# Performance work log

Measured on AMD Instinct MI355X. Metric: run time of the kernel, lower is better.

## Reference

```python
import jax, jax.numpy as jnp
import numpy as np

SEQ, SUB, B, V = 32, 16, 512, 258
U = SEQ // SUB
Z, CH, CO, DH = 512, 1024, 512, 1024


def _lstm_cell(x, h, c, Wi, Wh, bi, bh):
    # torch gate order: input, forget, cell, output
    g = x @ Wi + h @ Wh + bi + bh  # [B, 4H]
    i, f, gg, o = jnp.split(g, 4, axis=-1)
    c = jax.nn.sigmoid(f) * c + jax.nn.sigmoid(i) * jnp.tanh(gg)
    h = jax.nn.sigmoid(o) * jnp.tanh(c)
    return h, c


def _lstm2(xs, h1_0, p1, p2):
    # xs: [T,B,in]; h1_0: [B,H] layer-1 initial hidden.
    # Layer-2 hidden and both cell states start at zero (initialize_state in torch code).
    z0 = jnp.zeros_like(h1_0)
    def step(carry, x):
        h1, c1, h2, c2 = carry
        h1, c1 = _lstm_cell(x, h1, c1, *p1)
        h2, c2 = _lstm_cell(h1, h2, c2, *p2)
        return (h1, c1, h2, c2), h2
    _, hs = jax.lax.scan(step, (h1_0, z0, z0, z0), xs)
    return hs  # [T,B,H] top-layer hidden states


def setup_inputs() -> dict:
    key = jax.random.key(0)
    ks = iter(jax.random.split(key, 40))
    def w(shape, s=0.05):
        return jax.random.normal(next(ks), shape, dtype=jnp.float32) * s
    return {
        "z": jax.random.normal(next(ks), (B, Z), dtype=jnp.float32),
        "x": jax.random.uniform(next(ks), (SEQ, B, V), dtype=jnp.float32),
        "conductor_input": w((1, B, V)),
        "ci_W": w((Z, CH)), "ci_b": w((CH,)),
        "cW1i": w((V, 4 * CH)), "cW1h": w((CH, 4 * CH)), "cb1i": w((4 * CH,)), "cb1h": w((4 * CH,)),
        "cW2i": w((CH, 4 * CH)), "cW2h": w((CH, 4 * CH)), "cb2i": w((4 * CH,)), "cb2h": w((4 * CH,)),
        "co_W": w((CH, CO)), "co_b": w((CO,)),
        "di_W": w((CO, DH)), "di_b": w((DH,)),
        "dW1i": w((CO + V, 4 * DH)), "dW1h": w((DH, 4 * DH)), "db1i": w((4 * DH,)), "db1h": w((4 * DH,)),
        "dW2i": w((DH, 4 * DH)), "dW2h": w((DH, 4 * DH)), "db2i": w((4 * DH,)), "db2h": w((4 * DH,)),
        "fc_W": w((DH, V)), "fc_b": w((V,)),
    }


def reference(z, x, conductor_input, ci_W, ci_b, cW1i, cW1h, cb1i, cb1h, cW2i, cW2h, cb2i, cb2h, co_W, co_b, di_W, di_b, dW1i, dW1h, db1i, db1h, dW2i, dW2h, db2i, db2h, fc_W, fc_b):
    # --- conductor: 2-layer LSTM over U steps of a learned constant input ---
    h1 = jnp.tanh(z @ ci_W + ci_b)  # [B,CH] layer-1 init hidden
    cin = jnp.broadcast_to(conductor_input, (U, B, V))
    ch = _lstm2(cin, h1, (cW1i, cW1h, cb1i, cb1h), (cW2i, cW2h, cb2i, cb2h))  # [U,B,CH]
    c = ch @ co_W + co_b  # [U,B,CO]
    # --- decoder (teacher forcing): state resets each sub-sequence, so the U
    # segments of length SUB are independent given c -> vmap over segments ---
    sos = jnp.zeros((1, B, V), jnp.float32).at[:, :, 0].set(1.0)
    prev = jnp.concatenate([sos, x[:-1]], axis=0).reshape(U, SUB, B, V)
    cb = jnp.broadcast_to(c[:, None], (U, SUB, B, CO))
    dec_in = jnp.concatenate([cb, prev], axis=-1)  # [U,SUB,B,CO+V]
    def run_seg(xs, cj):
        h1_0 = jnp.tanh(cj @ di_W + di_b)  # [B,DH]
        return _lstm2(xs, h1_0, (dW1i, dW1h, db1i, db1h), (dW2i, dW2h, db2i, db2h))
    hs = jax.vmap(run_seg)(dec_in, c)  # [U,SUB,B,DH]
    logp = jax.nn.log_softmax(hs @ fc_W + fc_b, axis=-1)  # log(softmax(.)) fused
    return logp.reshape(SEQ, B, V).transpose(1, 0, 2)  # [B,SEQ,V]
```

## Files before the change

kernel.cpp:

```cpp
#include <hip/hip_runtime.h>
#include <cstddef>
#include <cstdint>


namespace {

typedef short s8v __attribute__((ext_vector_type(8)));
typedef float f4v __attribute__((ext_vector_type(4)));
typedef unsigned short ushort_t;

__device__ inline unsigned short f2bf(float f) {
    union { float f; unsigned u; } v; v.f = f;
    unsigned r = v.u + 0x7fff + ((v.u >> 16) & 1);
    return (unsigned short)(r >> 16);
}
__device__ inline float bf2f(ushort_t u) {
    union { unsigned u; float f; } v; v.u = ((unsigned)u) << 16; return v.f;
}
__device__ inline float sigm_f(float x) { return 1.f / (1.f + __expf(-x)); }
__device__ inline float tanh_f(float x) {
    const float e = __expf(2.f * fabsf(x));
    return copysignf(1.f - 2.f / (e + 1.f), x);
}

#define GLOAD_LDS(gp, lp)                                              \
    __builtin_amdgcn_global_load_lds(                                  \
        (const __attribute__((address_space(1))) void*)(gp),           \
        (__attribute__((address_space(3))) void*)(lp), 16, 0, 0)

__device__ __forceinline__ void gemm_core(
    const ushort_t* __restrict__ A1a, const ushort_t* __restrict__ A1b,
    int lda1, int K1, const ushort_t* __restrict__ B1t,
    const ushort_t* __restrict__ A2, int lda2, int K2,
    const ushort_t* __restrict__ B2t,
    int bm, int bn, ushort_t* lds, f4v acc[4][4])
{
    const int tid = threadIdx.x;
    const int wid = tid >> 6;
    const int lane = tid & 63;

    const int sr0 = wid * 16 + (lane >> 2);
    const int sr1 = sr0 + 64;
    const int rl0 = sr0 ^ ((sr0 >> 2) & 1);
    const int rl1 = sr1 ^ ((sr1 >> 2) & 1);
    const int c0 = (((lane & 3) ^ (rl0 & 3)) << 3);
    const int c1 = (((lane & 3) ^ (rl1 & 3)) << 3);
    const int ldst = wid * 512;

    auto arow = [&](const ushort_t* Aa, const ushort_t* Ab, int lda,
                    int r) -> const ushort_t* {
        return (Ab != nullptr && r >= 512) ? Ab + (size_t)(r - 512) * lda
                                           : Aa + (size_t)r * lda;
    };
    const ushort_t* a1r0 = arow(A1a, A1b, lda1, bm + rl0) + c0;
    const ushort_t* a1r1 = arow(A1a, A1b, lda1, bm + rl1) + c1;
    const ushort_t* b1r0 = B1t + (size_t)(bn + rl0) * K1 + c0;
    const ushort_t* b1r1 = B1t + (size_t)(bn + rl1) * K1 + c1;
    const int n1 = K1 >> 5, n2 = (B2t != nullptr) ? (K2 >> 5) : 0;
    const int nt = n1 + n2;
    const ushort_t* a2r0 = nullptr; const ushort_t* a2r1 = nullptr;
    const ushort_t* b2r0 = nullptr; const ushort_t* b2r1 = nullptr;
    if (n2 > 0) {
        a2r0 = A2 + (size_t)(bm + rl0) * lda2 + c0;
        a2r1 = A2 + (size_t)(bm + rl1) * lda2 + c1;
        b2r0 = B2t + (size_t)(bn + rl0) * K2 + c0;
        b2r1 = B2t + (size_t)(bn + rl1) * K2 + c1;
    }

    auto stage = [&](int idx, int buf) {
        ushort_t* Lb = lds + buf * 8192;
        const ushort_t *pa0, *pa1, *pb0, *pb1;
        if (idx < n1) {
            const int k0 = idx << 5;
            pa0 = a1r0 + k0; pa1 = a1r1 + k0; pb0 = b1r0 + k0; pb1 = b1r1 + k0;
        } else {
            const int k0 = (idx - n1) << 5;
            pa0 = a2r0 + k0; pa1 = a2r1 + k0; pb0 = b2r0 + k0; pb1 = b2r1 + k0;
        }
        GLOAD_LDS(pa0, Lb + ldst);
        GLOAD_LDS(pa1, Lb + 2048 + ldst);
        GLOAD_LDS(pb0, Lb + 4096 + ldst);
        GLOAD_LDS(pb1, Lb + 6144 + ldst);
    };

    const int wr = wid >> 1, wc = wid & 1;
    const int lrow = lane & 15, lkg = lane >> 4;
    int aoff[4], boff[4];
#pragma unroll
    for (int m = 0; m < 4; ++m) {
        const int r = wr * 64 + m * 16 + lrow;
        aoff[m] = (r ^ ((r >> 2) & 1)) * 32 + ((lkg ^ (r & 3)) << 3);
    }
#pragma unroll
    for (int n = 0; n < 4; ++n) {
        const int r = wc * 64 + n * 16 + lrow;
        boff[n] = 4096 + (r ^ ((r >> 2) & 1)) * 32 + ((lkg ^ (r & 3)) << 3);
    }

    stage(0, 0);
    stage(1, 1);
    int sbuf = 2, cbuf = 0;
    for (int t = 0; t < nt; ++t) {
        if (t == nt - 1) {
            asm volatile("s_waitcnt vmcnt(0)" ::: "memory");
        } else {
            asm volatile("s_waitcnt vmcnt(4)" ::: "memory");
        }
        __builtin_amdgcn_s_barrier();
        __builtin_amdgcn_sched_barrier(0);
        if (t + 2 < nt) {
            stage(t + 2, sbuf);
            sbuf = (sbuf == 2) ? 0 : sbuf + 1;
        }
        const ushort_t* L = lds + cbuf * 8192;
        s8v af[4], bv[4];
#pragma unroll
        for (int m = 0; m < 4; ++m) af[m] = *(const s8v*)(L + aoff[m]);
#pragma unroll
        for (int n = 0; n < 4; ++n) bv[n] = *(const s8v*)(L + boff[n]);
        __builtin_amdgcn_s_setprio(1);
#pragma unroll
        for (int m = 0; m < 4; ++m)
#pragma unroll
            for (int n = 0; n < 4; ++n)
                acc[m][n] = __builtin_amdgcn_mfma_f32_16x16x32_bf16(
                    af[m], bv[n], acc[m][n], 0, 0, 0);
        __builtin_amdgcn_s_setprio(0);
        cbuf = (cbuf == 2) ? 0 : cbuf + 1;
    }
}

template <int ACT>
__global__ __launch_bounds__(256) void plain_gemm(
    const ushort_t* __restrict__ A, int lda, int K,
    const ushort_t* __restrict__ Bt,
    const float* __restrict__ bias, int bias_n,
    float* __restrict__ C, ushort_t* __restrict__ Cbf, int N)
{
    __shared__ __align__(16) ushort_t lds[3 * 8192];
    const int bm = blockIdx.x * 128, bn = blockIdx.y * 128;
    f4v acc[4][4] = {};
    gemm_core(A, nullptr, lda, K, Bt, nullptr, 0, 0, nullptr, bm, bn, lds, acc);

    const int tid = threadIdx.x, wid = tid >> 6, lane = tid & 63;
    const int wr = wid >> 1, wc = wid & 1, lrow = lane & 15, lkg = lane >> 4;
#pragma unroll
    for (int m = 0; m < 4; ++m) {
        const int row0 = bm + wr * 64 + m * 16 + lkg * 4;
#pragma unroll
        for (int n = 0; n < 4; ++n) {
            const int col = bn + wc * 64 + n * 16 + lrow;
            const float bv = (bias != nullptr && col < bias_n) ? bias[col] : 0.f;
#pragma unroll
            for (int r = 0; r < 4; ++r) {
                float v = acc[m][n][r] + bv;
                if (ACT == 1) v = tanh_f(v);
                const size_t o = (size_t)(row0 + r) * N + col;
                if (C != nullptr) C[o] = v;
                if (Cbf != nullptr) Cbf[o] = f2bf(v);
            }
        }
    }
}

struct Prob {
    const ushort_t* A1a; const ushort_t* A1b; int lda1; int K1;
    const ushort_t* B1t;
    const ushort_t* A2; int lda2; int K2; const ushort_t* B2t;
    const ushort_t* Dbf;
    const float* bias;
    float* cst;
    ushort_t* hout;
    ushort_t* hs;
    int step_s;
};

__global__ __launch_bounds__(256) void lstm_step(Prob PA, int nxa, Prob PB,
                                                 int mshift)
{
    __shared__ __align__(16) ushort_t lds[3 * 8192];
    const int nblk = gridDim.x;
    const int wg = blockIdx.x;
    const int swz = (wg & 7) * (nblk >> 3) + (wg >> 3);
    const int nmb = 1 << mshift;
    const int nb = swz >> mshift;
    const int mb = swz & (nmb - 1);

    const bool isA = mb < nxa;
    const Prob& P = isA ? PA : PB;
    const int bm = (isA ? mb : mb - nxa) * 128;
    const int bn = nb * 128;

    f4v acc[4][4] = {};
    gemm_core(P.A1a, P.A1b, P.lda1, P.K1, P.B1t,
              P.A2, P.lda2, P.K2, P.B2t, bm, bn, lds, acc);

    const int tid = threadIdx.x, wid = tid >> 6, lane = tid & 63;
    const int wr = wid >> 1, wc = wid & 1, lrow = lane & 15, lkg = lane >> 4;
    const int colbase = bn + wc * 64;
    const int jb = (colbase >> 6) * 16 + lrow;

#pragma unroll
    for (int m = 0; m < 4; ++m) {
        const int row0 = bm + wr * 64 + m * 16 + lkg * 4;
#pragma unroll
        for (int r = 0; r < 4; ++r) {
            const int row = row0 + r;
            float g0 = acc[m][0][r], g1 = acc[m][1][r];
            float g2 = acc[m][2][r], g3 = acc[m][3][r];
            if (P.Dbf != nullptr) {
                const ushort_t* d = P.Dbf + (size_t)row * 4096 + colbase + lrow;
                g0 += bf2f(d[0]); g1 += bf2f(d[16]);
                g2 += bf2f(d[32]); g3 += bf2f(d[48]);
            }
            if (P.bias != nullptr) {
                const float* b = P.bias + colbase + lrow;
                g0 += b[0]; g1 += b[16]; g2 += b[32]; g3 += b[48];
            }
            const size_t ci = (size_t)row * 1024 + jb;
            const float cn = fmaf(sigm_f(g1), P.cst[ci], sigm_f(g0) * tanh_f(g2));
            const float hn = sigm_f(g3) * tanh_f(cn);
            P.cst[ci] = cn;
            const ushort_t hb = f2bf(hn);
            P.hout[ci] = hb;
            if (P.hs != nullptr) {
                size_t d;
                if (P.step_s >= 0) {
                    const int u = row >> 9, b = row & 511;
                    d = ((size_t)((u * 16 + P.step_s) * 512 + b) << 10) + jb;
                } else {
                    d = ci;
                }
                P.hs[d] = hb;
            }
        }
    }
}

template <int PERM>
__global__ __launch_bounds__(256) void transpose_to_bf16(
    const float* __restrict__ in, ushort_t* __restrict__ out,
    int K, int N, int Kp, int Np)
{
    __shared__ float tile[32][33];
    const int k0 = blockIdx.x * 32, n0 = blockIdx.y * 32;
    const int tx = threadIdx.x, ty = threadIdx.y;
#pragma unroll
    for (int q = 0; q < 4; ++q) {
        const int k = k0 + ty + 8 * q, n = n0 + tx;
        tile[ty + 8 * q][tx] = (k < K && n < N) ? in[(size_t)k * N + n] : 0.f;
    }
    __syncthreads();
#pragma unroll
    for (int q = 0; q < 4; ++q) {
        const int n = n0 + ty + 8 * q, k = k0 + tx;
        int np = n;
        if (PERM) np = ((n & 1023) >> 4) * 64 + (n >> 10) * 16 + (n & 15);
        out[(size_t)np * Kp + k] = f2bf(tile[tx][ty + 8 * q]);
    }
}

__global__ void convert_pad_bf16(const float* __restrict__ in,
                                 ushort_t* __restrict__ out,
                                 int K, int Kp, int total)
{
    const int idx = blockIdx.x * 256 + threadIdx.x;
    if (idx >= total) return;
    const int r = idx / Kp, k = idx - r * Kp;
    out[idx] = (k < K) ? f2bf(in[(size_t)r * K + k]) : (ushort_t)0;
}

__global__ void sos_init_bf16(ushort_t* __restrict__ sos)
{
    const int i = blockIdx.x * 256 + threadIdx.x;
    if (i < 512 * 288) sos[i] = ((i % 288) == 0) ? (ushort_t)0x3F80 : (ushort_t)0;
}

__global__ void permute_bias(const float* __restrict__ b1,
                             const float* __restrict__ b2,
                             float* __restrict__ out)
{
    const int c = blockIdx.x * 256 + threadIdx.x;
    if (c >= 4096) return;
    const int g = (c >> 4) & 3;
    const int j = (c >> 6) * 16 + (c & 15);
    out[c] = b1[g * 1024 + j] + b2[g * 1024 + j];
}

__global__ __launch_bounds__(256) void logsoftmax_kernel(
    const float* __restrict__ logits, float* __restrict__ out)
{
    const int row = blockIdx.x;
    const int tid = threadIdx.x;
    const float* L = logits + (size_t)row * 384;
    const int t = row >> 9;
    const int b = row & 511;
    float* O = out + ((size_t)b * 32 + t) * 258;

    const float x0 = L[tid];
    const float x1 = (tid < 2) ? L[256 + tid] : -1e30f;

    __shared__ float sm[4];
    float m = fmaxf(x0, x1);
#pragma unroll
    for (int off = 32; off > 0; off >>= 1) m = fmaxf(m, __shfl_down(m, off));
    if ((tid & 63) == 0) sm[tid >> 6] = m;
    __syncthreads();
    m = fmaxf(fmaxf(sm[0], sm[1]), fmaxf(sm[2], sm[3]));
    __syncthreads();

    float s = expf(x0 - m) + ((tid < 2) ? expf(x1 - m) : 0.f);
#pragma unroll
    for (int off = 32; off > 0; off >>= 1) s += __shfl_down(s, off);
    if ((tid & 63) == 0) sm[tid >> 6] = s;
    __syncthreads();
    s = sm[0] + sm[1] + sm[2] + sm[3];

    const float lse = m + logf(s);
    O[tid] = x0 - lse;
    if (tid < 2) O[256 + tid] = x1 - lse;
}

}

extern "C" void kernel_launch(void* const* d_in, const int* in_sizes, int n_in,
                              void* d_out, int out_size, void* d_ws, size_t ws_size,
                              hipStream_t stream)
{
    (void)in_sizes; (void)n_in; (void)out_size; (void)ws_size;

    const float* z    = (const float*)d_in[0];
    const float* x    = (const float*)d_in[1];
    const float* cin  = (const float*)d_in[2];
    const float* ciW  = (const float*)d_in[3];
    const float* cib  = (const float*)d_in[4];
    const float* cW1i = (const float*)d_in[5];
    const float* cW1h = (const float*)d_in[6];
    const float* cb1i = (const float*)d_in[7];
    const float* cb1h = (const float*)d_in[8];
    const float* cW2i = (const float*)d_in[9];
    const float* cW2h = (const float*)d_in[10];
    const float* cb2i = (const float*)d_in[11];
    const float* cb2h = (const float*)d_in[12];
    const float* coW  = (const float*)d_in[13];
    const float* cob  = (const float*)d_in[14];
    const float* diW  = (const float*)d_in[15];
    const float* dib  = (const float*)d_in[16];
    const float* dW1i = (const float*)d_in[17];
    const float* dW1h = (const float*)d_in[18];
    const float* db1i = (const float*)d_in[19];
    const float* db1h = (const float*)d_in[20];
    const float* dW2i = (const float*)d_in[21];
    const float* dW2h = (const float*)d_in[22];
    const float* db2i = (const float*)d_in[23];
    const float* db2h = (const float*)d_in[24];
    const float* fcW  = (const float*)d_in[25];
    const float* fcb  = (const float*)d_in[26];
    float* out = (float*)d_out;

    char* wsp = (char*)d_ws;
    size_t off = 0;
    auto allocf = [&](size_t n) { float* p = (float*)(wsp + off); off += n * 4; return p; };
    auto allocb = [&](size_t n) { ushort_t* p = (ushort_t*)(wsp + off); off += n * 2; return p; };

    float* cst = allocf((size_t)3 * 1024 * 1024 + 64);
    float* c1c = cst;
    float* c2c = cst + (size_t)512 * 1024;
    float* c1d = cst + (size_t)1024 * 1024;
    float* c2d = cst + (size_t)2 * 1024 * 1024;
    float* pb1c = allocf(4096);
    float* pb2c = allocf(4096);
    float* pb1d = allocf(4096);
    float* pb2d = allocf(4096);
    float* logits = allocf((size_t)16384 * 384);

    ushort_t* h2z  = allocb((size_t)2 * (512 + 1024) * 1024);
    ushort_t* hc2A = h2z;
    ushort_t* hc2B = h2z + (size_t)512 * 1024;
    ushort_t* h2dA = h2z + (size_t)2 * 512 * 1024;
    ushort_t* h2dB = h2z + (size_t)(2 * 512 + 1024) * 1024;

    ushort_t* hc1A = allocb((size_t)512 * 1024);
    ushort_t* hc1B = allocb((size_t)512 * 1024);
    ushort_t* h1dA = allocb((size_t)1024 * 1024);
    ushort_t* h1dB = allocb((size_t)1024 * 1024);

    ushort_t* zbf    = allocb((size_t)512 * 512);
    ushort_t* cinbf  = allocb((size_t)512 * 288);
    ushort_t* sosbf  = allocb((size_t)512 * 288);
    ushort_t* xbf    = allocb((size_t)16384 * 288);
    ushort_t* chbf   = allocb((size_t)1024 * 1024);
    ushort_t* ccode  = allocb((size_t)1024 * 512);
    ushort_t* cpre   = allocb((size_t)1024 * 4096);
    ushort_t* xW1c   = allocb((size_t)512 * 4096);
    ushort_t* hsbf   = allocb((size_t)16384 * 1024);

    ushort_t* ciWt  = allocb((size_t)1024 * 512);
    ushort_t* cW1it = allocb((size_t)4096 * 288);
    ushort_t* cW1ht = allocb((size_t)4096 * 1024);
    ushort_t* cW2it = allocb((size_t)4096 * 1024);
    ushort_t* cW2ht = allocb((size_t)4096 * 1024);
    ushort_t* coWt  = allocb((size_t)512 * 1024);
    ushort_t* dtopt = allocb((size_t)4096 * 512);
    ushort_t* dbott = allocb((size_t)4096 * 288);
    ushort_t* diWt  = allocb((size_t)1024 * 512);
    ushort_t* dW1ht = allocb((size_t)4096 * 1024);
    ushort_t* dW2it = allocb((size_t)4096 * 1024);
    ushort_t* dW2ht = allocb((size_t)4096 * 1024);
    ushort_t* fcWt  = allocb((size_t)384 * 1024);

    hipMemsetAsync(cst, 0, (size_t)3 * 1024 * 1024 * 4, stream);
    hipMemsetAsync(h2z, 0, (size_t)2 * (512 + 1024) * 1024 * 2, stream);

    auto transp = [&](const float* in, ushort_t* o, int K, int N, int Kp, int Np, int perm) {
        dim3 g(Kp / 32, Np / 32), b(32, 8);
        if (perm) transpose_to_bf16<1><<<g, b, 0, stream>>>(in, o, K, N, Kp, Np);
        else      transpose_to_bf16<0><<<g, b, 0, stream>>>(in, o, K, N, Kp, Np);
    };
    transp(ciW, ciWt, 512, 1024, 512, 1024, 0);
    transp(cW1i, cW1it, 258, 4096, 288, 4096, 1);
    transp(cW1h, cW1ht, 1024, 4096, 1024, 4096, 1);
    transp(cW2i, cW2it, 1024, 4096, 1024, 4096, 1);
    transp(cW2h, cW2ht, 1024, 4096, 1024, 4096, 1);
    transp(coW, coWt, 1024, 512, 1024, 512, 0);
    transp(dW1i, dtopt, 512, 4096, 512, 4096, 1);
    transp(dW1i + (size_t)512 * 4096, dbott, 258, 4096, 288, 4096, 1);
    transp(diW, diWt, 512, 1024, 512, 1024, 0);
    transp(dW1h, dW1ht, 1024, 4096, 1024, 4096, 1);
    transp(dW2i, dW2it, 1024, 4096, 1024, 4096, 1);
    transp(dW2h, dW2ht, 1024, 4096, 1024, 4096, 1);
    transp(fcW, fcWt, 1024, 258, 1024, 384, 0);

    auto convert = [&](const float* in, ushort_t* o, int K, int Kp, int R) {
        const int total = R * Kp;
        convert_pad_bf16<<<dim3((total + 255) / 256), 256, 0, stream>>>(in, o, K, Kp, total);
    };
    convert(z, zbf, 512, 512, 512);
    convert(cin, cinbf, 258, 288, 512);
    convert(x, xbf, 258, 288, 16384);
    sos_init_bf16<<<dim3((512 * 288 + 255) / 256), 256, 0, stream>>>(sosbf);
    permute_bias<<<16, 256, 0, stream>>>(cb1i, cb1h, pb1c);
    permute_bias<<<16, 256, 0, stream>>>(cb2i, cb2h, pb2c);
    permute_bias<<<16, 256, 0, stream>>>(db1i, db1h, pb1d);
    permute_bias<<<16, 256, 0, stream>>>(db2i, db2h, pb2d);

    auto gemm = [&](int act, const ushort_t* A, int lda, int K, const ushort_t* Bt,
                    const float* bias, int bias_n,
                    float* C, ushort_t* Cbf, int M, int N) {
        dim3 g(M / 128, N / 128);
        if (act) plain_gemm<1><<<g, 256, 0, stream>>>(A, lda, K, Bt, bias, bias_n, C, Cbf, N);
        else     plain_gemm<0><<<g, 256, 0, stream>>>(A, lda, K, Bt, bias, bias_n, C, Cbf, N);
    };

    gemm(1, zbf, 512, 512, ciWt, cib, 1024, nullptr, hc1A, 512, 1024);
    gemm(0, cinbf, 288, 288, cW1it, pb1c, 4096, nullptr, xW1c, 512, 4096);

    ushort_t* HC1[2] = {hc1A, hc1B};
    ushort_t* HC2[2] = {hc2A, hc2B};
    for (int k = 0; k <= 2; ++k) {
        Prob pa{}, pb{};
        int nxa = 0, nxb = 0;
        if (k < 2) {
            pa = {HC1[k & 1], nullptr, 1024, 1024, cW1ht,
                  nullptr, 0, 0, nullptr,
                  xW1c, nullptr, c1c, HC1[(k + 1) & 1], nullptr, -1};
            nxa = 4;
        }
        if (k >= 1) {
            pb = {HC1[k & 1], nullptr, 1024, 1024, cW2it,
                  HC2[k & 1], 1024, 1024, cW2ht,
                  nullptr, pb2c, c2c, HC2[(k + 1) & 1],
                  chbf + (size_t)(k - 1) * 512 * 1024, -1};
            nxb = 4;
        }
        const int nmb = nxa + nxb;
        const int mshift = (nmb == 4) ? 2 : 3;
        lstm_step<<<dim3(nmb * 32), 256, 0, stream>>>(pa, nxa, pb, mshift);
    }

    gemm(0, chbf, 1024, 1024, coWt, cob, 512, nullptr, ccode, 1024, 512);
    gemm(0, ccode, 512, 512, dtopt, pb1d, 4096, nullptr, cpre, 1024, 4096);
    gemm(1, ccode, 512, 512, diWt, dib, 1024, nullptr, h1dA, 1024, 1024);

    ushort_t* H1[2] = {h1dA, h1dB};
    ushort_t* H2[2] = {h2dA, h2dB};
    for (int k = 0; k <= 16; ++k) {
        Prob pa{}, pb{};
        int nxa = 0, nxb = 0;
        if (k < 16) {
            const ushort_t* plo = (k == 0) ? sosbf : (xbf + (size_t)(k - 1) * 512 * 288);
            const ushort_t* phi = xbf + (size_t)(15 + k) * 512 * 288;
            pa = {plo, phi, 288, 288, dbott,
                  H1[k & 1], 1024, 1024, dW1ht,
                  cpre, nullptr, c1d, H1[(k + 1) & 1], nullptr, -1};
            nxa = 8;
        }
        if (k >= 1) {
            pb = {H1[k & 1], nullptr, 1024, 1024, dW2it,
                  H2[k & 1], 1024, 1024, dW2ht,
                  nullptr, pb2d, c2d, H2[(k + 1) & 1], hsbf, k - 1};
            nxb = 8;
        }
        const int nmb = nxa + nxb;
        const int mshift = (nmb == 8) ? 3 : 4;
        lstm_step<<<dim3(nmb * 32), 256, 0, stream>>>(pa, nxa, pb, mshift);
    }

    gemm(0, hsbf, 1024, 1024, fcWt, fcb, 258, logits, nullptr, 16384, 384);
    logsoftmax_kernel<<<dim3(16384), 256, 0, stream>>>(logits, out);
}
```

Baseline: 1.108 ms.

## Enlarge GEMM tiles to 128x256 with K=64 stages and XOR-swizzled LDS

Changes the shared GEMM core from 128x128 tiles with a K step of 32 to 128x256 tiles with a K step of 64. Staging uses row-wise global-to-LDS loads and an 8-chunk XOR swizzle, and the LSTM and plain GEMM launches halve their column-block count. The padded K of the 258-wide inputs grows from 288 to 320, and the logits width from 384 to 512, so dimensions stay multiples of the new tile sizes. This aims to raise MFMA work per LDS load and cut redundant A-tile fetches. In exchange, LDS use and register pressure rise (launch bounds of one block), grids shrink so fewer CUs are busy on the small recurrent steps, and the padding adds wasted work.

```diff
diff --git a/kernel.cpp b/kernel.cpp
--- a/kernel.cpp
+++ b/kernel.cpp
@@ -27,119 +27,114 @@
     __builtin_amdgcn_global_load_lds(                                  \
         (const __attribute__((address_space(1))) void*)(gp),           \
         (__attribute__((address_space(3))) void*)(lp), 16, 0, 0)
+
+constexpr int kBufElems = 24576;
 
 __device__ __forceinline__ void gemm_core(
     const ushort_t* __restrict__ A1a, const ushort_t* __restrict__ A1b,
     int lda1, int K1, const ushort_t* __restrict__ B1t,
     const ushort_t* __restrict__ A2, int lda2, int K2,
     const ushort_t* __restrict__ B2t,
-    int bm, int bn, ushort_t* lds, f4v acc[4][4])
+    int bm, int bn, ushort_t* lds, f4v acc[4][8])
 {
     const int tid = threadIdx.x;
     const int wid = tid >> 6;
     const int lane = tid & 63;
 
-    const int sr0 = wid * 16 + (lane >> 2);
-    const int sr1 = sr0 + 64;
-    const int rl0 = sr0 ^ ((sr0 >> 2) & 1);
-    const int rl1 = sr1 ^ ((sr1 >> 2) & 1);
-    const int c0 = (((lane & 3) ^ (rl0 & 3)) << 3);
-    const int c1 = (((lane & 3) ^ (rl1 & 3)) << 3);
-    const int ldst = wid * 512;
-
-    auto arow = [&](const ushort_t* Aa, const ushort_t* Ab, int lda,
-                    int r) -> const ushort_t* {
-        return (Ab != nullptr && r >= 512) ? Ab + (size_t)(r - 512) * lda
-                                           : Aa + (size_t)r * lda;
-    };
-    const ushort_t* a1r0 = arow(A1a, A1b, lda1, bm + rl0) + c0;
-    const ushort_t* a1r1 = arow(A1a, A1b, lda1, bm + rl1) + c1;
-    const ushort_t* b1r0 = B1t + (size_t)(bn + rl0) * K1 + c0;
-    const ushort_t* b1r1 = B1t + (size_t)(bn + rl1) * K1 + c1;
-    const int n1 = K1 >> 5, n2 = (B2t != nullptr) ? (K2 >> 5) : 0;
+    const int srow8 = lane >> 3;
+    const int schunk = (lane & 7) ^ srow8;
+
+    const int n1 = K1 >> 6;
+    const int n2 = (B2t != nullptr) ? (K2 >> 6) : 0;
     const int nt = n1 + n2;
-    const ushort_t* a2r0 = nullptr; const ushort_t* a2r1 = nullptr;
-    const ushort_t* b2r0 = nullptr; const ushort_t* b2r1 = nullptr;
+
+    const ushort_t* Ab1 = (A1b != nullptr && bm >= 512)
+                              ? A1b + (size_t)(bm - 512) * lda1
+                              : A1a + (size_t)bm * lda1;
+    const ushort_t* pA1 = Ab1 + (size_t)(wid * 32 + srow8) * lda1 + schunk * 8;
+    const ushort_t* pB1 = B1t + (size_t)(bn + wid * 64 + srow8) * K1 + schunk * 8;
+    const ushort_t* pA2 = nullptr;
+    const ushort_t* pB2 = nullptr;
     if (n2 > 0) {
-        a2r0 = A2 + (size_t)(bm + rl0) * lda2 + c0;
-        a2r1 = A2 + (size_t)(bm + rl1) * lda2 + c1;
-        b2r0 = B2t + (size_t)(bn + rl0) * K2 + c0;
-        b2r1 = B2t + (size_t)(bn + rl1) * K2 + c1;
+        pA2 = A2 + (size_t)(bm + wid * 32 + srow8) * lda2 + schunk * 8;
+        pB2 = B2t + (size_t)(bn + wid * 64 + srow8) * K2 + schunk * 8;
     }
 
     auto stage = [&](int idx, int buf) {
-        ushort_t* Lb = lds + buf * 8192;
-        const ushort_t *pa0, *pa1, *pb0, *pb1;
-        if (idx < n1) {
-            const int k0 = idx << 5;
-            pa0 = a1r0 + k0; pa1 = a1r1 + k0; pb0 = b1r0 + k0; pb1 = b1r1 + k0;
-        } else {
-            const int k0 = (idx - n1) << 5;
-            pa0 = a2r0 + k0; pa1 = a2r1 + k0; pb0 = b2r0 + k0; pb1 = b2r1 + k0;
-        }
-        GLOAD_LDS(pa0, Lb + ldst);
-        GLOAD_LDS(pa1, Lb + 2048 + ldst);
-        GLOAD_LDS(pb0, Lb + 4096 + ldst);
-        GLOAD_LDS(pb1, Lb + 6144 + ldst);
+        ushort_t* Lb = lds + buf * kBufElems;
+        const ushort_t *pa, *pb;
+        size_t la, lb;
+        if (idx < n1) { pa = pA1 + (idx << 6); pb = pB1 + (idx << 6); la = lda1; lb = K1; }
+        else { const int i2 = idx - n1; pa = pA2 + (i2 << 6); pb = pB2 + (i2 << 6); la = lda2; lb = K2; }
+#pragma unroll
+        for (int j = 0; j < 4; ++j)
+            GLOAD_LDS(pa + (size_t)(j * 8) * la, Lb + (wid * 32 + j * 8) * 64);
+#pragma unroll
+        for (int j = 0; j < 8; ++j)
+            GLOAD_LDS(pb + (size_t)(j * 8) * lb, Lb + 8192 + (wid * 64 + j * 8) * 64);
     };
 
     const int wr = wid >> 1, wc = wid & 1;
     const int lrow = lane & 15, lkg = lane >> 4;
-    int aoff[4], boff[4];
+    int aoff[4][2], boff[8][2];
 #pragma unroll
     for (int m = 0; m < 4; ++m) {
         const int r = wr * 64 + m * 16 + lrow;
-        aoff[m] = (r ^ ((r >> 2) & 1)) * 32 + ((lkg ^ (r & 3)) << 3);
-    }
-#pragma unroll
-    for (int n = 0; n < 4; ++n) {
-        const int r = wc * 64 + n * 16 + lrow;
-        boff[n] = 4096 + (r ^ ((r >> 2) & 1)) * 32 + ((lkg ^ (r & 3)) << 3);
+#pragma unroll
+        for (int s = 0; s < 2; ++s)
+            aoff[m][s] = r * 64 + (((s * 4 + lkg) ^ (r & 7)) << 3);
+    }
+#pragma unroll
+    for (int n = 0; n < 8; ++n) {
+        const int r = wc * 128 + n * 16 + lrow;
+#pragma unroll
+        for (int s = 0; s < 2; ++s)
+            boff[n][s] = 8192 + r * 64 + (((s * 4 + lkg) ^ (r & 7)) << 3);
     }
 
     stage(0, 0);
-    stage(1, 1);
+    if (nt > 1) stage(1, 1);
     int sbuf = 2, cbuf = 0;
     for (int t = 0; t < nt; ++t) {
-        if (t == nt - 1) {
-            asm volatile("s_waitcnt vmcnt(0)" ::: "memory");
-        } else {
-            asm volatile("s_waitcnt vmcnt(4)" ::: "memory");
-        }
+        if (t + 1 < nt) asm volatile("s_waitcnt vmcnt(12)" ::: "memory");
+        else            asm volatile("s_waitcnt vmcnt(0)" ::: "memory");
         __builtin_amdgcn_s_barrier();
         __builtin_amdgcn_sched_barrier(0);
         if (t + 2 < nt) {
             stage(t + 2, sbuf);
             sbuf = (sbuf == 2) ? 0 : sbuf + 1;
         }
-        const ushort_t* L = lds + cbuf * 8192;
-        s8v af[4], bv[4];
-#pragma unroll
-        for (int m = 0; m < 4; ++m) af[m] = *(const s8v*)(L + aoff[m]);
-#pragma unroll
-        for (int n = 0; n < 4; ++n) bv[n] = *(const s8v*)(L + boff[n]);
-        __builtin_amdgcn_s_setprio(1);
-#pragma unroll
-        for (int m = 0; m < 4; ++m)
-#pragma unroll
-            for (int n = 0; n < 4; ++n)
-                acc[m][n] = __builtin_amdgcn_mfma_f32_16x16x32_bf16(
-                    af[m], bv[n], acc[m][n], 0, 0, 0);
-        __builtin_amdgcn_s_setprio(0);
+        const ushort_t* L = lds + cbuf * kBufElems;
+#pragma unroll
+        for (int s = 0; s < 2; ++s) {
+            s8v a[4], b[8];
+#pragma unroll
+            for (int m = 0; m < 4; ++m) a[m] = *(const s8v*)(L + aoff[m][s]);
+#pragma unroll
+            for (int n = 0; n < 8; ++n) b[n] = *(const s8v*)(L + boff[n][s]);
+            __builtin_amdgcn_s_setprio(1);
+#pragma unroll
+            for (int m = 0; m < 4; ++m)
+#pragma unroll
+                for (int n = 0; n < 8; ++n)
+                    acc[m][n] = __builtin_amdgcn_mfma_f32_16x16x32_bf16(
+                        a[m], b[n], acc[m][n], 0, 0, 0);
+            __builtin_amdgcn_s_setprio(0);
+        }
         cbuf = (cbuf == 2) ? 0 : cbuf + 1;
     }
 }
 
 template <int ACT>
-__global__ __launch_bounds__(256) void plain_gemm(
+__global__ __launch_bounds__(256, 1) void plain_gemm(
     const ushort_t* __restrict__ A, int lda, int K,
     const ushort_t* __restrict__ Bt,
     const float* __restrict__ bias, int bias_n,
     float* __restrict__ C, ushort_t* __restrict__ Cbf, int N)
 {
-    __shared__ __align__(16) ushort_t lds[3 * 8192];
-    const int bm = blockIdx.x * 128, bn = blockIdx.y * 128;
-    f4v acc[4][4] = {};
+    __shared__ __align__(16) ushort_t lds[3 * kBufElems];
+    const int bm = blockIdx.x * 128, bn = blockIdx.y * 256;
+    f4v acc[4][8] = {};
     gemm_core(A, nullptr, lda, K, Bt, nullptr, 0, 0, nullptr, bm, bn, lds, acc);
 
     const int tid = threadIdx.x, wid = tid >> 6, lane = tid & 63;
@@ -148,8 +143,8 @@
     for (int m = 0; m < 4; ++m) {
         const int row0 = bm + wr * 64 + m * 16 + lkg * 4;
 #pragma unroll
-        for (int n = 0; n < 4; ++n) {
-            const int col = bn + wc * 64 + n * 16 + lrow;
+        for (int n = 0; n < 8; ++n) {
+            const int col = bn + wc * 128 + n * 16 + lrow;
             const float bv = (bias != nullptr && col < bias_n) ? bias[col] : 0.f;
 #pragma unroll
             for (int r = 0; r < 4; ++r) {
@@ -175,10 +170,10 @@
     int step_s;
 };
 
-__global__ __launch_bounds__(256) void lstm_step(Prob PA, int nxa, Prob PB,
-                                                 int mshift)
-{
-    __shared__ __align__(16) ushort_t lds[3 * 8192];
+__global__ __launch_bounds__(256, 1) void lstm_step(Prob PA, int nxa, Prob PB,
+                                                    int mshift)
+{
+    __shared__ __align__(16) ushort_t lds[3 * kBufElems];
     const int nblk = gridDim.x;
     const int wg = blockIdx.x;
     const int swz = (wg & 7) * (nblk >> 3) + (wg >> 3);
@@ -189,49 +184,52 @@
     const bool isA = mb < nxa;
     const Prob& P = isA ? PA : PB;
     const int bm = (isA ? mb : mb - nxa) * 128;
-    const int bn = nb * 128;
-
-    f4v acc[4][4] = {};
+    const int bn = nb * 256;
+
+    f4v acc[4][8] = {};
     gemm_core(P.A1a, P.A1b, P.lda1, P.K1, P.B1t,
               P.A2, P.lda2, P.K2, P.B2t, bm, bn, lds, acc);
 
     const int tid = threadIdx.x, wid = tid >> 6, lane = tid & 63;
     const int wr = wid >> 1, wc = wid & 1, lrow = lane & 15, lkg = lane >> 4;
-    const int colbase = bn + wc * 64;
-    const int jb = (colbase >> 6) * 16 + lrow;
-
-#pragma unroll
-    for (int m = 0; m < 4; ++m) {
-        const int row0 = bm + wr * 64 + m * 16 + lkg * 4;
-#pragma unroll
-        for (int r = 0; r < 4; ++r) {
-            const int row = row0 + r;
-            float g0 = acc[m][0][r], g1 = acc[m][1][r];
-            float g2 = acc[m][2][r], g3 = acc[m][3][r];
-            if (P.Dbf != nullptr) {
-                const ushort_t* d = P.Dbf + (size_t)row * 4096 + colbase + lrow;
-                g0 += bf2f(d[0]); g1 += bf2f(d[16]);
-                g2 += bf2f(d[32]); g3 += bf2f(d[48]);
-            }
-            if (P.bias != nullptr) {
-                const float* b = P.bias + colbase + lrow;
-                g0 += b[0]; g1 += b[16]; g2 += b[32]; g3 += b[48];
-            }
-            const size_t ci = (size_t)row * 1024 + jb;
-            const float cn = fmaf(sigm_f(g1), P.cst[ci], sigm_f(g0) * tanh_f(g2));
-            const float hn = sigm_f(g3) * tanh_f(cn);
-            P.cst[ci] = cn;
-            const ushort_t hb = f2bf(hn);
-            P.hout[ci] = hb;
-            if (P.hs != nullptr) {
-                size_t d;
-                if (P.step_s >= 0) {
-                    const int u = row >> 9, b = row & 511;
-                    d = ((size_t)((u * 16 + P.step_s) * 512 + b) << 10) + jb;
-                } else {
-                    d = ci;
+
+#pragma unroll
+    for (int nn = 0; nn < 2; ++nn) {
+        const int colbase = bn + wc * 128 + nn * 64;
+        const int jb = (colbase >> 6) * 16 + lrow;
+#pragma unroll
+        for (int m = 0; m < 4; ++m) {
+            const int row0 = bm + wr * 64 + m * 16 + lkg * 4;
+#pragma unroll
+            for (int r = 0; r < 4; ++r) {
+                const int row = row0 + r;
+                float g0 = acc[m][nn * 4 + 0][r], g1 = acc[m][nn * 4 + 1][r];
+                float g2 = acc[m][nn * 4 + 2][r], g3 = acc[m][nn * 4 + 3][r];
+                if (P.Dbf != nullptr) {
+                    const ushort_t* d = P.Dbf + (size_t)row * 4096 + colbase + lrow;
+                    g0 += bf2f(d[0]); g1 += bf2f(d[16]);
+                    g2 += bf2f(d[32]); g3 += bf2f(d[48]);
                 }
-                P.hs[d] = hb;
+                if (P.bias != nullptr) {
+                    const float* b = P.bias + colbase + lrow;
+                    g0 += b[0]; g1 += b[16]; g2 += b[32]; g3 += b[48];
+                }
+                const size_t ci = (size_t)row * 1024 + jb;
+                const float cn = fmaf(sigm_f(g1), P.cst[ci], sigm_f(g0) * tanh_f(g2));
+                const float hn = sigm_f(g3) * tanh_f(cn);
+                P.cst[ci] = cn;
+                const ushort_t hb = f2bf(hn);
+                P.hout[ci] = hb;
+                if (P.hs != nullptr) {
+                    size_t d;
+                    if (P.step_s >= 0) {
+                        const int u = row >> 9, b = row & 511;
+                        d = ((size_t)((u * 16 + P.step_s) * 512 + b) << 10) + jb;
+                    } else {
+                        d = ci;
+                    }
+                    P.hs[d] = hb;
+                }
             }
         }
     }
@@ -273,7 +271,7 @@
 __global__ void sos_init_bf16(ushort_t* __restrict__ sos)
 {
     const int i = blockIdx.x * 256 + threadIdx.x;
-    if (i < 512 * 288) sos[i] = ((i % 288) == 0) ? (ushort_t)0x3F80 : (ushort_t)0;
+    if (i < 512 * 320) sos[i] = ((i % 320) == 0) ? (ushort_t)0x3F80 : (ushort_t)0;
 }
 
 __global__ void permute_bias(const float* __restrict__ b1,
@@ -292,7 +290,7 @@
 {
     const int row = blockIdx.x;
     const int tid = threadIdx.x;
-    const float* L = logits + (size_t)row * 384;
+    const float* L = logits + (size_t)row * 512;
     const int t = row >> 9;
     const int b = row & 511;
     float* O = out + ((size_t)b * 32 + t) * 258;
@@ -372,7 +370,7 @@
     float* pb2c = allocf(4096);
     float* pb1d = allocf(4096);
     float* pb2d = allocf(4096);
-    float* logits = allocf((size_t)16384 * 384);
+    float* logits = allocf((size_t)16384 * 512);
 
     ushort_t* h2z  = allocb((size_t)2 * (512 + 1024) * 1024);
     ushort_t* hc2A = h2z;
@@ -386,9 +384,9 @@
     ushort_t* h1dB = allocb((size_t)1024 * 1024);
 
     ushort_t* zbf    = allocb((size_t)512 * 512);
-    ushort_t* cinbf  = allocb((size_t)512 * 288);
-    ushort_t* sosbf  = allocb((size_t)512 * 288);
-    ushort_t* xbf    = allocb((size_t)16384 * 288);
+    ushort_t* cinbf  = allocb((size_t)512 * 320);
+    ushort_t* sosbf  = allocb((size_t)512 * 320);
+    ushort_t* xbf    = allocb((size_t)16384 * 320);
     ushort_t* chbf   = allocb((size_t)1024 * 1024);
     ushort_t* ccode  = allocb((size_t)1024 * 512);
     ushort_t* cpre   = allocb((size_t)1024 * 4096);
@@ -396,18 +394,18 @@
     ushort_t* hsbf   = allocb((size_t)16384 * 1024);
 
     ushort_t* ciWt  = allocb((size_t)1024 * 512);
-    ushort_t* cW1it = allocb((size_t)4096 * 288);
+    ushort_t* cW1it = allocb((size_t)4096 * 320);
     ushort_t* cW1ht = allocb((size_t)4096 * 1024);
     ushort_t* cW2it = allocb((size_t)4096 * 1024);
     ushort_t* cW2ht = allocb((size_t)4096 * 1024);
     ushort_t* coWt  = allocb((size_t)512 * 1024);
     ushort_t* dtopt = allocb((size_t)4096 * 512);
-    ushort_t* dbott = allocb((size_t)4096 * 288);
+    ushort_t* dbott = allocb((size_t)4096 * 320);
     ushort_t* diWt  = allocb((size_t)1024 * 512);
     ushort_t* dW1ht = allocb((size_t)4096 * 1024);
     ushort_t* dW2it = allocb((size_t)4096 * 1024);
     ushort_t* dW2ht = allocb((size_t)4096 * 1024);
-    ushort_t* fcWt  = allocb((size_t)384 * 1024);
+    ushort_t* fcWt  = allocb((size_t)512 * 1024);
 
     hipMemsetAsync(cst, 0, (size_t)3 * 1024 * 1024 * 4, stream);
     hipMemsetAsync(h2z, 0, (size_t)2 * (512 + 1024) * 1024 * 2, stream);
@@ -418,27 +416,27 @@
         else      transpose_to_bf16<0><<<g, b, 0, stream>>>(in, o, K, N, Kp, Np);
     };
     transp(ciW, ciWt, 512, 1024, 512, 1024, 0);
-    transp(cW1i, cW1it, 258, 4096, 288, 4096, 1);
+    transp(cW1i, cW1it, 258, 4096, 320, 4096, 1);
     transp(cW1h, cW1ht, 1024, 4096, 1024, 4096, 1);
     transp(cW2i, cW2it, 1024, 4096, 1024, 4096, 1);
     transp(cW2h, cW2ht, 1024, 4096, 1024, 4096, 1);
     transp(coW, coWt, 1024, 512, 1024, 512, 0);
     transp(dW1i, dtopt, 512, 4096, 512, 4096, 1);
-    transp(dW1i + (size_t)512 * 4096, dbott, 258, 4096, 288, 4096, 1);
+    transp(dW1i + (size_t)512 * 4096, dbott, 258, 4096, 320, 4096, 1);
     transp(diW, diWt, 512, 1024, 512, 1024, 0);
     transp(dW1h, dW1ht, 1024, 4096, 1024, 4096, 1);
     transp(dW2i, dW2it, 1024, 4096, 1024, 4096, 1);
     transp(dW2h, dW2ht, 1024, 4096, 1024, 4096, 1);
-    transp(fcW, fcWt, 1024, 258, 1024, 384, 0);
+    transp(fcW, fcWt, 1024, 258, 1024, 512, 0);
 
     auto convert = [&](const float* in, ushort_t* o, int K, int Kp, int R) {
         const int total = R * Kp;
         convert_pad_bf16<<<dim3((total + 255) / 256), 256, 0, stream>>>(in, o, K, Kp, total);
     };
     convert(z, zbf, 512, 512, 512);
-    convert(cin, cinbf, 258, 288, 512);
-    convert(x, xbf, 258, 288, 16384);
-    sos_init_bf16<<<dim3((512 * 288 + 255) / 256), 256, 0, stream>>>(sosbf);
+    convert(cin, cinbf, 258, 320, 512);
+    convert(x, xbf, 258, 320, 16384);
+    sos_init_bf16<<<dim3((512 * 320 + 255) / 256), 256, 0, stream>>>(sosbf);
     permute_bias<<<16, 256, 0, stream>>>(cb1i, cb1h, pb1c);
     permute_bias<<<16, 256, 0, stream>>>(cb2i, cb2h, pb2c);
     permute_bias<<<16, 256, 0, stream>>>(db1i, db1h, pb1d);
@@ -447,13 +445,13 @@
     auto gemm = [&](int act, const ushort_t* A, int lda, int K, const ushort_t* Bt,
                     const float* bias, int bias_n,
                     float* C, ushort_t* Cbf, int M, int N) {
-        dim3 g(M / 128, N / 128);
+        dim3 g(M / 128, N / 256);
         if (act) plain_gemm<1><<<g, 256, 0, stream>>>(A, lda, K, Bt, bias, bias_n, C, Cbf, N);
         else     plain_gemm<0><<<g, 256, 0, stream>>>(A, lda, K, Bt, bias, bias_n, C, Cbf, N);
     };
 
     gemm(1, zbf, 512, 512, ciWt, cib, 1024, nullptr, hc1A, 512, 1024);
-    gemm(0, cinbf, 288, 288, cW1it, pb1c, 4096, nullptr, xW1c, 512, 4096);
+    gemm(0, cinbf, 320, 320, cW1it, pb1c, 4096, nullptr, xW1c, 512, 4096);
 
     ushort_t* HC1[2] = {hc1A, hc1B};
     ushort_t* HC2[2] = {hc2A, hc2B};
@@ -475,7 +473,7 @@
         }
         const int nmb = nxa + nxb;
         const int mshift = (nmb == 4) ? 2 : 3;
-        lstm_step<<<dim3(nmb * 32), 256, 0, stream>>>(pa, nxa, pb, mshift);
+        lstm_step<<<dim3(nmb * 16), 256, 0, stream>>>(pa, nxa, pb, mshift);
     }
 
     gemm(0, chbf, 1024, 1024, coWt, cob, 512, nullptr, ccode, 1024, 512);
@@ -488,9 +486,9 @@
         Prob pa{}, pb{};
         int nxa = 0, nxb = 0;
         if (k < 16) {
-            const ushort_t* plo = (k == 0) ? sosbf : (xbf + (size_t)(k - 1) * 512 * 288);
-            const ushort_t* phi = xbf + (size_t)(15 + k) * 512 * 288;
-            pa = {plo, phi, 288, 288, dbott,
+            const ushort_t* plo = (k == 0) ? sosbf : (xbf + (size_t)(k - 1) * 512 * 320);
+            const ushort_t* phi = xbf + (size_t)(15 + k) * 512 * 320;
+            pa = {plo, phi, 320, 320, dbott,
                   H1[k & 1], 1024, 1024, dW1ht,
                   cpre, nullptr, c1d, H1[(k + 1) & 1], nullptr, -1};
             nxa = 8;
@@ -503,9 +501,9 @@
         }
         const int nmb = nxa + nxb;
         const int mshift = (nmb == 8) ? 3 : 4;
-        lstm_step<<<dim3(nmb * 32), 256, 0, stream>>>(pa, nxa, pb, mshift);
-    }
-
-    gemm(0, hsbf, 1024, 1024, fcWt, fcb, 258, logits, nullptr, 16384, 384);
+        lstm_step<<<dim3(nmb * 16), 256, 0, stream>>>(pa, nxa, pb, mshift);
+    }
+
+    gemm(0, hsbf, 1024, 1024, fcWt, fcb, 258, logits, nullptr, 16384, 512);
     logsoftmax_kernel<<<dim3(16384), 256, 0, stream>>>(logits, out);
 }
```

Measured after the change: 1.299 ms. +17.2%, slower.
